# Kernel optimization log

Measured on AMD Instinct MI355X. Metric: run time of the kernel, lower is better.

The kernel has to match this reference:

```python
import jax, jax.numpy as jnp
import numpy as np

N = 13627
E = 504378
D = 500


def _seg_softmax(e, seg, n):
    m = jax.ops.segment_max(e, seg, num_segments=n)
    ex = jnp.exp(e - m[seg])
    s = jax.ops.segment_sum(ex, seg, num_segments=n)
    return ex / (s[seg] + 1e-16)


def _gatv2(x, src, dst, Wl, Wr, att, b, n):
    # PyG GATv2Conv (heads=1): message = Wl x_src; score uses Wl x_src + Wr x_dst
    xl = x @ Wl                                   # [N, F]
    xr = x @ Wr                                   # [N, F]
    e = jax.nn.leaky_relu(xl[src] + xr[dst], 0.2) @ att   # [E]
    a = _seg_softmax(e, dst, n)                   # segment softmax over targets
    out = jax.ops.segment_sum(a[:, None] * xl[src], dst, num_segments=n)
    return out + b


def setup_inputs() -> dict:
    key = jax.random.key(0)
    ks = jax.random.split(key, 24)
    s = 0.05
    inp = {
        'x': jax.random.normal(ks[0], (N, D), dtype=jnp.float32),
        'edge_index': jax.random.randint(ks[1], (2, E), 0, N),
        'neg_edge_index': jax.random.randint(ks[2], (2, E), 0, N),
        'Wl1': jax.random.normal(ks[3], (D, 300)) * s,
        'Wr1': jax.random.normal(ks[4], (D, 300)) * s,
        'att1': jax.random.normal(ks[5], (300,)) * s,
        'b1': jnp.zeros((300,)),
        'Wl2': jax.random.normal(ks[6], (300, 100)) * s,
        'Wr2': jax.random.normal(ks[7], (300, 100)) * s,
        'att2': jax.random.normal(ks[8], (100,)) * s,
        'b2': jnp.zeros((100,)),
        'Wl3': jax.random.normal(ks[9], (100, 1)) * s,
        'Wr3': jax.random.normal(ks[10], (100, 1)) * s,
        'att3': jax.random.normal(ks[11], (1,)) * s,
        'b3': jnp.zeros((1,)),
        'W_lin1': jax.random.normal(ks[12], (D, 100)) * s,
        'b_lin1': jnp.zeros((100,)),
        'W_lin2': jax.random.normal(ks[13], (D, 100)) * s,
        'b_lin2': jnp.zeros((100,)),
        'c1': jnp.array([0.5], dtype=jnp.float32),
        'c2': jnp.array([0.5], dtype=jnp.float32),
    }
    return inp


def reference(x, edge_index, neg_edge_index, Wl1, Wr1, att1, b1, Wl2, Wr2, att2, b2,
              Wl3, Wr3, att3, b3, W_lin1, b_lin1, W_lin2, b_lin2, c1, c2):
    # eval mode: dropout / dropout_adj are identity
    loops = jnp.arange(N)
    src = jnp.concatenate([edge_index[0], loops])   # GATv2Conv adds self loops
    dst = jnp.concatenate([edge_index[1], loops])

    h1 = jax.nn.relu(_gatv2(x, src, dst, Wl1, Wr1, att1, b1, N))
    h2 = jax.nn.relu(_gatv2(h1, src, dst, Wl2, Wr2, att2, b2, N))

    xo = h2 + jax.nn.relu(x @ W_lin1 + b_lin1)
    z = h2 + jax.nn.relu(x @ W_lin2 + b_lin2)

    # link-prediction reconstruction loss
    pos_s = jnp.sum(z[edge_index[0]] * z[edge_index[1]], axis=1)
    pos_loss = -jnp.mean(jnp.log(jax.nn.sigmoid(pos_s) + 1e-15))
    neg_s = jnp.sum(z[neg_edge_index[0]] * z[neg_edge_index[1]], axis=1)
    neg_loss = -jnp.mean(jnp.log(1.0 - jax.nn.sigmoid(neg_s) + 1e-15))
    r_loss = pos_loss + neg_loss

    out = _gatv2(xo, src, dst, Wl3, Wr3, att3, b3, N)   # [N, 1]
    return out, r_loss, c1, c2
```

## Files before the change

kernel.cpp:

```cpp
#include <hip/hip_runtime.h>
#include <hip/hip_bf16.h>

#define NODES 13627
#define DIM   500

typedef short short8 __attribute__((ext_vector_type(8)));
typedef float f32x4 __attribute__((ext_vector_type(4)));
typedef float floatx2 __attribute__((ext_vector_type(2)));

__device__ inline float wave_reduce_sum(float v) {
#pragma unroll
    for (int o = 32; o > 0; o >>= 1) v += __shfl_xor(v, o, 64);
    return v;
}

__device__ inline void store_v(float* p, float v) { *p = v; }
__device__ inline void store_v(__hip_bfloat16* p, float v) { *p = __float2bfloat16(v); }

__device__ inline float blo(unsigned w) { unsigned t = w << 16;        return __builtin_bit_cast(float, t); }
__device__ inline float bhi(unsigned w) { unsigned t = w & 0xffff0000u; return __builtin_bit_cast(float, t); }

__device__ inline unsigned char to_fp8(float v) {
    int r = __builtin_amdgcn_cvt_pk_fp8_f32(v, v, 0, false);
    return (unsigned char)(r & 0xff);
}

__device__ inline unsigned pk2bf(float a, float b) {
    unsigned la = (unsigned)__builtin_bit_cast(unsigned short, __float2bfloat16(a));
    unsigned hb = (unsigned)__builtin_bit_cast(unsigned short, __float2bfloat16(b));
    return la | (hb << 16);
}

template <int CTRL>
__device__ inline float dpp_add_step(float v) {
    int s = __builtin_amdgcn_update_dpp(0, __builtin_bit_cast(int, v), CTRL, 0xf, 0xf, true);
    return v + __builtin_bit_cast(float, s);
}
__device__ inline float quad16_reduce(float v) {
    v = dpp_add_step<0x128>(v);
    v = dpp_add_step<0x124>(v);
    v = dpp_add_step<0x4E>(v);
    v = dpp_add_step<0xB1>(v);
    return v;
}

struct b4 { __hip_bfloat16 a, b, c, d; };

__global__ __launch_bounds__(1024) void scan_kernel(int* __restrict__ cnt_cur,
                                                    int* __restrict__ off, int n) {
    __shared__ int wsum[16];
    const int tid = threadIdx.x, lane = tid & 63, w = tid >> 6;
    int carry = 0;
    for (int base = 0; base < n; base += 1024) {
        int i = base + tid;
        int v = (i < n) ? cnt_cur[i] : 0;
        int s = v;
#pragma unroll
        for (int o = 1; o < 64; o <<= 1) {
            int t = __shfl_up(s, o, 64);
            if (lane >= o) s += t;
        }
        if (lane == 63) wsum[w] = s;
        __syncthreads();
        if (w == 0 && lane < 16) {
            int x = wsum[lane];
            int sx = x;
#pragma unroll
            for (int o = 1; o < 16; o <<= 1) {
                int t = __shfl_up(sx, o, 64);
                if (lane >= o) sx += t;
            }
            wsum[lane] = sx;
        }
        __syncthreads();
        int wo = (w == 0) ? 0 : wsum[w - 1];
        int total = wsum[15];
        int excl = carry + wo + (s - v);
        if (i < n) { off[i] = excl; cnt_cur[i] = excl; }
        carry += total;
        __syncthreads();
    }
    if (tid == 0) off[n] = carry;
}

__global__ __launch_bounds__(256) void scatter_kernel(const int* __restrict__ src,
                                                      const int* __restrict__ dst,
                                                      int* __restrict__ cur,
                                                      int* __restrict__ ssrc, int E) {
    int i = blockIdx.x * blockDim.x + threadIdx.x;
    if (i < E) {
        int p = atomicAdd(&cur[dst[i]], 1);
        ssrc[p] = src[i];
    }
}

__global__ __launch_bounds__(256) void convert_all_kernel(
    const float* __restrict__ x,
    const float* __restrict__ Wl1, const float* __restrict__ Wr1,
    const float* __restrict__ Wl2, const float* __restrict__ Wr2,
    const float* __restrict__ Ws1, const float* __restrict__ Ws2,
    const float* __restrict__ bs1, const float* __restrict__ bs2,
    __hip_bfloat16* __restrict__ WcT, __hip_bfloat16* __restrict__ W2T,
    float* __restrict__ bcat, __hip_bfloat16* __restrict__ xb,
    const int* __restrict__ dst, int* __restrict__ cnt, int E, int M) {
    int i = blockIdx.x * 256 + threadIdx.x;
    if (i < E) atomicAdd(&cnt[dst[i]], 1);
    if (i < 327680) {
        int n = i >> 9, k = i & 511;
        float v = 0.f;
        if (k < 500) {
            if (n < 300) v = Wl1[k * 300 + n];
            else if (n < 600) v = Wr1[k * 300 + n - 300];
        }
        WcT[i] = __float2bfloat16(v);
    } else if (i < 409600) {
        int j = i - 327680;
        int n = j / 320, k = j - n * 320;
        float v = 0.f;
        if (k < 300) {
            if (n < 100) v = Wl2[k * 100 + n];
            else if (n < 200) v = Wr2[k * 100 + n - 100];
        }
        W2T[j] = __float2bfloat16(v);
    } else if (i < 540672) {
        int j = i - 409600;
        int n = j >> 9, k = j & 511;
        float v = 0.f;
        if (k < 500) {
            if (n < 100) v = Ws1[k * 100 + n];
            else if (n < 200) v = Ws2[k * 100 + n - 100];
        }
        WcT[327680 + j] = __float2bfloat16(v);
    } else if (i < 540928) {
        int n = i - 540672;
        float v = 0.f;
        if (n < 100) v = bs1[n];
        else if (n < 200) v = bs2[n - 100];
        bcat[n] = v;
    } else {
        int j = i - 540928;
        if (j >= M * 128) return;
        int m = j >> 7, k = (j & 127) << 2;
        b4 o;
        if (k < 500) {
            float4 v = *(const float4*)(x + (size_t)m * 500 + k);
            o.a = __float2bfloat16(v.x); o.b = __float2bfloat16(v.y);
            o.c = __float2bfloat16(v.z); o.d = __float2bfloat16(v.w);
        } else {
            o.a = o.b = o.c = o.d = __float2bfloat16(0.f);
        }
        *(b4*)(xb + (size_t)m * 512 + k) = o;
    }
}

template <int EPI, typename TC>
__global__ __launch_bounds__(256) void mfma_gemm(
    const __hip_bfloat16* __restrict__ A, const __hip_bfloat16* __restrict__ BT,
    TC* __restrict__ C, const float* __restrict__ bias, const float* __restrict__ h2,
    unsigned char* __restrict__ p8, __hip_bfloat16* __restrict__ pb,
    int M, int Kp, int Nn, int ldc) {
    __shared__ short AsF[8 * 64 * 8];
    __shared__ short BsF[4 * 64 * 8];
    const int t = threadIdx.x;
    const int w = t >> 6, lane = t & 63;
    const int c = t & 3, rr = t >> 2;

    const int nwg = gridDim.x * gridDim.y;
    int id = blockIdx.y * gridDim.x + blockIdx.x;
    {
        const int xcd = id & 7, idx = id >> 3;
        const int qq = nwg >> 3, r8 = nwg & 7;
        id = (xcd < r8 ? xcd * (qq + 1) : r8 * (qq + 1) + (xcd - r8) * qq) + idx;
    }
    const int m0 = (id / gridDim.x) * 128, n0 = (id % gridDim.x) * 64;

    f32x4 acc[2][4];
#pragma unroll
    for (int i = 0; i < 2; i++)
#pragma unroll
        for (int j = 0; j < 4; j++) acc[i][j] = (f32x4){0.f, 0.f, 0.f, 0.f};

    for (int k0 = 0; k0 < Kp; k0 += 32) {
#pragma unroll
        for (int r = 0; r < 2; r++) {
            int m = r * 64 + rr;
            int gm = m0 + m; if (gm >= M) gm = M - 1;
            float4 v = *(const float4*)(A + (size_t)gm * Kp + k0 + c * 8);
            int mi = m >> 4, sl = m & 15;
            *(float4*)(&AsF[(mi * 64 + c * 16 + sl) * 8]) = v;
        }
        {
            int n = rr;
            float4 v = *(const float4*)(BT + (size_t)(n0 + n) * Kp + k0 + c * 8);
            int ni = n >> 4, sl = n & 15;
            *(float4*)(&BsF[(ni * 64 + c * 16 + sl) * 8]) = v;
        }
        __syncthreads();
        short8 a0 = *(const short8*)(&AsF[((w * 2 + 0) * 64 + lane) * 8]);
        short8 a1 = *(const short8*)(&AsF[((w * 2 + 1) * 64 + lane) * 8]);
#pragma unroll
        for (int j = 0; j < 4; j++) {
            short8 b = *(const short8*)(&BsF[(j * 64 + lane) * 8]);
            acc[0][j] = __builtin_amdgcn_mfma_f32_16x16x32_bf16(a0, b, acc[0][j], 0, 0, 0);
            acc[1][j] = __builtin_amdgcn_mfma_f32_16x16x32_bf16(a1, b, acc[1][j], 0, 0, 0);
        }
        __syncthreads();
    }

    const int q = lane >> 4, sl = lane & 15;
#pragma unroll
    for (int i = 0; i < 2; i++) {
#pragma unroll
        for (int j = 0; j < 4; j++) {
#pragma unroll
            for (int reg = 0; reg < 4; reg++) {
                int gm = m0 + w * 32 + i * 16 + q * 4 + reg;
                int gn = n0 + j * 16 + sl;
                if (gm >= M) continue;
                float v = acc[i][j][reg];
                if constexpr (EPI == 1) {
                    if (gn < 300)       p8[(size_t)gm * 304 + gn] = to_fp8(v);
                    else if (gn < 600)  pb[(size_t)gm * 320 + (gn - 300)] = __float2bfloat16(v);
                    else if (gn < 620)  pb[(size_t)gm * 320 + (gn - 300)] = __float2bfloat16(0.f);
                    else if (gn < 624)  p8[(size_t)gm * 304 + (gn - 320)] = 0;
                    else if (gn >= 640 && gn < 840) {
                        int cn = gn - 640;
                        ((float*)C)[(size_t)gm * 200 + cn] = fmaxf(v + bias[cn], 0.f);
                    }
                } else if constexpr (EPI == 2) {
                    if (gn < 100)       p8[(size_t)gm * 112 + gn] = to_fp8(v);
                    else if (gn < 200)  pb[(size_t)gm * 128 + (gn - 100)] = __float2bfloat16(v);
                    else if (gn < 212)  p8[(size_t)gm * 112 + (gn - 100)] = 0;
                    else if (gn < 240)  pb[(size_t)gm * 128 + (gn - 112)] = __float2bfloat16(0.f);
                } else {
                    store_v(&C[(size_t)gm * ldc + gn], v);
                }
            }
        }
    }
}

template <int F, int NJ, int SL8, int SRB, int SOUT, int JSL, typename TOUT, bool FUSE>
__global__ __launch_bounds__(64, 4) void gat_f8_kernel(
    const unsigned char* __restrict__ xl8, const __hip_bfloat16* __restrict__ xrb,
    const float* __restrict__ att, const float* __restrict__ bias,
    const int* __restrict__ off, const int* __restrict__ ssrc,
    TOUT* __restrict__ out,
    const float* __restrict__ wpre, unsigned char* __restrict__ z8o,
    float* __restrict__ xl3, float* __restrict__ xr3,
    const float* __restrict__ wl3, const float* __restrict__ wr3, int n) {
    const int lane = threadIdx.x;
    const int sl = lane & 15, q = lane >> 4;
    const int wid = blockIdx.x;

    floatx2 attv[NJ * 2], xrv[NJ * 2], acc[NJ * 2];
    const unsigned* xru = (const unsigned*)xrb + (size_t)wid * (SRB / 2);
#pragma unroll
    for (int j = 0; j < NJ; j++) {
        const int f0 = sl * 4 + j * 64;
        if (f0 < F) {
            float4 a4 = *(const float4*)(att + f0);
            attv[j * 2 + 0] = (floatx2){a4.x, a4.y};
            attv[j * 2 + 1] = (floatx2){a4.z, a4.w};
        } else {
            attv[j * 2 + 0] = (floatx2){0.f, 0.f};
            attv[j * 2 + 1] = (floatx2){0.f, 0.f};
        }
        unsigned u0 = __builtin_nontemporal_load(xru + (f0 >> 1));
        unsigned u1 = __builtin_nontemporal_load(xru + (f0 >> 1) + 1);
        xrv[j * 2 + 0] = (floatx2){blo(u0), bhi(u0)};
        xrv[j * 2 + 1] = (floatx2){blo(u1), bhi(u1)};
        acc[j * 2 + 0] = (floatx2){0.f, 0.f};
        acc[j * 2 + 1] = (floatx2){0.f, 0.f};
    }

    const int s0 = off[wid], s1 = off[wid + 1];
    const int eb = s0 - 1;
    const int ee = s1;
    float den = 0.f;
    const int myoff = sl * 4;

    int srcB;
    unsigned u[NJ];
    {
        int eq0 = eb + q;
        int srcA = wid;
        if (eq0 >= s0 && eq0 < ee) srcA = __builtin_nontemporal_load(ssrc + eq0);
        int eq1 = eb + 4 + q;
        srcB = wid;
        if (eq1 >= s0 && eq1 < ee) srcB = __builtin_nontemporal_load(ssrc + eq1);
        const unsigned char* row = xl8 + (size_t)srcA * SL8;
#pragma unroll
        for (int j = 0; j < NJ; j++) {
            const bool ld = (j < NJ - 1) || (sl < JSL);
            u[j] = ld ? *(const unsigned*)(row + myoff + j * 64) : 0u;
        }
    }

    float p_pend = 0.f, gate = 0.f;
    unsigned u_pend[NJ];
#pragma unroll
    for (int j = 0; j < NJ; j++) u_pend[j] = 0u;

    for (int e0 = eb; e0 < ee; e0 += 4) {
        int srcC = wid;
        {
            int eq2 = e0 + 8 + q;
            if (eq2 >= s0 && eq2 < ee) srcC = __builtin_nontemporal_load(ssrc + eq2);
        }
        unsigned un[NJ];
        {
            const unsigned char* row1 = xl8 + (size_t)srcB * SL8;
#pragma unroll
            for (int j = 0; j < NJ; j++) {
                const bool ld = (j < NJ - 1) || (sl < JSL);
                un[j] = ld ? *(const unsigned*)(row1 + myoff + j * 64) : 0u;
            }
        }
        {
            float pp = quad16_reduce(p_pend);
            float ex = gate * __expf(pp);
            den += ex;
            floatx2 ex2 = (floatx2){ex, ex};
#pragma unroll
            for (int j = 0; j < NJ; j++) {
                floatx2 lo = __builtin_amdgcn_cvt_pk_f32_fp8((int)u_pend[j], false);
                floatx2 hi = __builtin_amdgcn_cvt_pk_f32_fp8((int)u_pend[j], true);
                acc[j * 2 + 0] += ex2 * lo;
                acc[j * 2 + 1] += ex2 * hi;
            }
        }
        {
            floatx2 p2 = (floatx2){0.f, 0.f};
#pragma unroll
            for (int j = 0; j < NJ; j++) {
                floatx2 lo = __builtin_amdgcn_cvt_pk_f32_fp8((int)u[j], false);
                floatx2 hi = __builtin_amdgcn_cvt_pk_f32_fp8((int)u[j], true);
                floatx2 s0v = lo + xrv[j * 2 + 0];
                floatx2 s1v = hi + xrv[j * 2 + 1];
                floatx2 g0 = __builtin_elementwise_max(s0v, 0.2f * s0v);
                floatx2 g1 = __builtin_elementwise_max(s1v, 0.2f * s1v);
                p2 += attv[j * 2 + 0] * g0;
                p2 += attv[j * 2 + 1] * g1;
            }
            p_pend = p2.x + p2.y;
            gate = ((e0 + q) < ee) ? 1.f : 0.f;
        }
#pragma unroll
        for (int j = 0; j < NJ; j++) { u_pend[j] = u[j]; u[j] = un[j]; }
        srcB = srcC;
    }
    {
        float pp = quad16_reduce(p_pend);
        float ex = gate * __expf(pp);
        den += ex;
        floatx2 ex2 = (floatx2){ex, ex};
#pragma unroll
        for (int j = 0; j < NJ; j++) {
            floatx2 lo = __builtin_amdgcn_cvt_pk_f32_fp8((int)u_pend[j], false);
            floatx2 hi = __builtin_amdgcn_cvt_pk_f32_fp8((int)u_pend[j], true);
            acc[j * 2 + 0] += ex2 * lo;
            acc[j * 2 + 1] += ex2 * hi;
        }
    }

    float* af = (float*)acc;
#pragma unroll
    for (int o = 16; o <= 32; o <<= 1) {
        den += __shfl_xor(den, o, 64);
#pragma unroll
        for (int i = 0; i < NJ * 4; i++) af[i] += __shfl_xor(af[i], o, 64);
    }

    if (q == 0) {
        const float inv = 1.f / (den + 1e-16f);
        if constexpr (FUSE) {
            float pl = 0.f, pr = 0.f;
#pragma unroll
            for (int j = 0; j < NJ; j++) {
                const int f0 = sl * 4 + j * 64;
#pragma unroll
                for (int cc = 0; cc < 4; cc++) {
                    const int f = f0 + cc;
                    if (f < F) {
                        float h2v = fmaxf(af[j * 4 + cc] * inv + bias[f], 0.f);
                        float preA = wpre[(size_t)wid * 200 + f];
                        float preB = wpre[(size_t)wid * 200 + 100 + f];
                        float xov = preA + h2v;
                        z8o[(size_t)wid * 128 + f] = to_fp8(preB + h2v);
                        pl += xov * wl3[f];
                        pr += xov * wr3[f];
                    } else {
                        z8o[(size_t)wid * 128 + f] = 0;
                    }
                }
            }
            pl = quad16_reduce(pl);
            pr = quad16_reduce(pr);
            if (sl == 0) { xl3[wid] = pl; xr3[wid] = pr; }
        } else {
#pragma unroll
            for (int j = 0; j < NJ; j++) {
                const int f0 = sl * 4 + j * 64;
                if (f0 >= SOUT) continue;
                float r[4];
#pragma unroll
                for (int cc = 0; cc < 4; cc++) {
                    const int f = f0 + cc;
                    float v = 0.f;
                    if (f < F) v = fmaxf(af[j * 4 + cc] * inv + bias[f], 0.f);
                    r[cc] = v;
                }
                if constexpr (sizeof(TOUT) == 4) {
                    *(float4*)((float*)out + (size_t)wid * SOUT + f0) =
                        make_float4(r[0], r[1], r[2], r[3]);
                } else {
                    unsigned* op = (unsigned*)out + (size_t)wid * (SOUT / 2) + (f0 >> 1);
                    op[0] = pk2bf(r[0], r[1]);
                    op[1] = pk2bf(r[2], r[3]);
                }
            }
        }
    }
}

__global__ __launch_bounds__(256) void gat3_kernel(
    const float* __restrict__ xl3, const float* __restrict__ xr3,
    const float* __restrict__ att3, const float* __restrict__ b3,
    const int* __restrict__ off, const int* __restrict__ ssrc,
    float* __restrict__ out, int n,
    const float* __restrict__ part, int nb,
    const float* __restrict__ c1, const float* __restrict__ c2, int E) {
    __shared__ float sp[4], sn[4];
    if (blockIdx.x == gridDim.x - 1) {
        const int tid = threadIdx.x, lane = tid & 63, w = tid >> 6;
        float p = 0.f, q2 = 0.f;
        for (int i = tid; i < nb; i += 256) { p += part[i]; q2 += part[nb + i]; }
        p = wave_reduce_sum(p);
        q2 = wave_reduce_sum(q2);
        if (lane == 0) { sp[w] = p; sn[w] = q2; }
        __syncthreads();
        if (tid == 0) {
            float tp = sp[0] + sp[1] + sp[2] + sp[3];
            float tq = sn[0] + sn[1] + sn[2] + sn[3];
            out[n]     = -(tp + tq) / (float)E;
            out[n + 1] = c1[0];
            out[n + 2] = c2[0];
        }
        return;
    }
    const int wid = blockIdx.x * 4 + (threadIdx.x >> 6);
    const int lane = threadIdx.x & 63;
    if (wid >= n) return;
    const float xrv = xr3[wid];
    const float att = att3[0];
    float num = 0.f, den = 0.f;
    const int s0 = off[wid], s1 = off[wid + 1];
    for (int e = s0 - 1 + lane; e < s1; e += 64) {
        int src = (e < s0) ? wid : ssrc[e];
        float xlv = xl3[src];
        float t = xlv + xrv;
        float g = t > 0.f ? t : 0.2f * t;
        float ex = __expf(g * att);
        den += ex;
        num += ex * xlv;
    }
    num = wave_reduce_sum(num);
    den = wave_reduce_sum(den);
    if (lane == 0) out[wid] = num / (den + 1e-16f) + b3[0];
}

__global__ __launch_bounds__(256) void loss_kernel(
    const unsigned char* __restrict__ z8, const int* __restrict__ pos,
    const int* __restrict__ neg, float* __restrict__ part, int nb, int E) {
    const int lane = threadIdx.x & 63;
    const int sl = lane & 15;
    const int wlocal = threadIdx.x >> 6;
    const int q = lane >> 4;
    const int nq = gridDim.x * 16;
    const int qid = (blockIdx.x * 4 + wlocal) * 4 + q;
    const int total = 2 * E;
    float psum = 0.f, nsum = 0.f;

    for (int base = qid; base < total; base += 4 * nq) {
        uint2 au[4], bu[4];
        bool act[4], isN[4];
#pragma unroll
        for (int s = 0; s < 4; s++) {
            int it = base + s * nq;
            act[s] = it < total;
            int itc = act[s] ? it : 0;
            isN[s] = itc >= E;
            int e = isN[s] ? itc - E : itc;
            const int* ei = isN[s] ? neg : pos;
            int u = ei[e], v = ei[E + e];
            au[s] = *(const uint2*)(z8 + (size_t)u * 128 + sl * 8);
            bu[s] = *(const uint2*)(z8 + (size_t)v * 128 + sl * 8);
        }
#pragma unroll
        for (int s = 0; s < 4; s++) {
            floatx2 a0 = __builtin_amdgcn_cvt_pk_f32_fp8((int)au[s].x, false);
            floatx2 a1 = __builtin_amdgcn_cvt_pk_f32_fp8((int)au[s].x, true);
            floatx2 a2 = __builtin_amdgcn_cvt_pk_f32_fp8((int)au[s].y, false);
            floatx2 a3 = __builtin_amdgcn_cvt_pk_f32_fp8((int)au[s].y, true);
            floatx2 b0 = __builtin_amdgcn_cvt_pk_f32_fp8((int)bu[s].x, false);
            floatx2 b1 = __builtin_amdgcn_cvt_pk_f32_fp8((int)bu[s].x, true);
            floatx2 b2 = __builtin_amdgcn_cvt_pk_f32_fp8((int)bu[s].y, false);
            floatx2 b3 = __builtin_amdgcn_cvt_pk_f32_fp8((int)bu[s].y, true);
            float p = a0.x * b0.x + a0.y * b0.y + a1.x * b1.x + a1.y * b1.y
                    + a2.x * b2.x + a2.y * b2.y + a3.x * b3.x + a3.y * b3.y;
            p = quad16_reduce(p);
            if (sl == 0 && act[s]) {
                float sig = __builtin_amdgcn_rcpf(1.f + __expf(-p));
                if (isN[s]) nsum += __logf(1.f - sig + 1e-15f);
                else        psum += __logf(sig + 1e-15f);
            }
        }
    }
    float pw = wave_reduce_sum(psum);
    float nw = wave_reduce_sum(nsum);
    __shared__ float sp[4], sn[4];
    if (lane == 0) { sp[wlocal] = pw; sn[wlocal] = nw; }
    __syncthreads();
    if (threadIdx.x == 0) {
        part[blockIdx.x]      = sp[0] + sp[1] + sp[2] + sp[3];
        part[nb + blockIdx.x] = sn[0] + sn[1] + sn[2] + sn[3];
    }
}

extern "C" void kernel_launch(void* const* d_in, const int* in_sizes, int n_in,
                              void* d_out, int out_size, void* d_ws, size_t ws_size,
                              hipStream_t stream) {
    const float* x      = (const float*)d_in[0];
    const int*   ei     = (const int*)d_in[1];
    const int*   nei    = (const int*)d_in[2];
    const float* Wl1    = (const float*)d_in[3];
    const float* Wr1    = (const float*)d_in[4];
    const float* att1   = (const float*)d_in[5];
    const float* b1     = (const float*)d_in[6];
    const float* Wl2    = (const float*)d_in[7];
    const float* Wr2    = (const float*)d_in[8];
    const float* att2   = (const float*)d_in[9];
    const float* b2     = (const float*)d_in[10];
    const float* Wl3    = (const float*)d_in[11];
    const float* Wr3    = (const float*)d_in[12];
    const float* att3   = (const float*)d_in[13];
    const float* b3     = (const float*)d_in[14];
    const float* Wlin1  = (const float*)d_in[15];
    const float* blin1  = (const float*)d_in[16];
    const float* Wlin2  = (const float*)d_in[17];
    const float* blin2  = (const float*)d_in[18];
    const float* c1     = (const float*)d_in[19];
    const float* c2     = (const float*)d_in[20];
    float* out = (float*)d_out;

    const int E = in_sizes[1] / 2;
    const int N = NODES;
    const int LOSS_BLOCKS = 4096;

    char* ws = (char*)d_ws;
    unsigned char*  xl8  = (unsigned char*)(ws + 0);
    unsigned char*  xl28 = (unsigned char*)(ws + 0);
    __hip_bfloat16* xrb  = (__hip_bfloat16*)(ws + 4194304);
    __hip_bfloat16* xr2b = (__hip_bfloat16*)(ws + 4194304);
    unsigned char*  z8   = (unsigned char*)(ws + 9645312);
    __hip_bfloat16* h1b  = (__hip_bfloat16*)(ws + 12915712);
    __hip_bfloat16* xb   = (__hip_bfloat16*)(ws + 21637120);
    __hip_bfloat16* WcT  = (__hip_bfloat16*)(ws + 35591168);
    __hip_bfloat16* W2T  = (__hip_bfloat16*)(ws + 36508672);
    float*          bcat = (float*)(ws + 36672512);
    float*          xl3  = (float*)(ws + 36673536);
    float*          xr3  = (float*)(ws + 36728064);
    int*            ioff = (int*)(ws + 36782592);
    int*            cur  = (int*)(ws + 36837376);
    int*            ssrc = (int*)(ws + 36892160);
    float*          part = (float*)(ws + 38909952);
    float*          wpre = (float*)(ws + 39000064);

    hipMemsetAsync(cur, 0, sizeof(int) * N, stream);

    convert_all_kernel<<<(540928 + N * 128 + 255) / 256, 256, 0, stream>>>(
        x, Wl1, Wr1, Wl2, Wr2, Wlin1, Wlin2, blin1, blin2,
        WcT, W2T, bcat, xb, ei + E, cur, E, N);

    scan_kernel<<<1, 1024, 0, stream>>>(cur, ioff, N);
    scatter_kernel<<<(E + 255) / 256, 256, 0, stream>>>(ei, ei + E, cur, ssrc, E);

    mfma_gemm<1, float><<<dim3(14, 107), 256, 0, stream>>>(
        xb, WcT, wpre, bcat, nullptr, xl8, xrb, N, 512, 896, 200);
    gat_f8_kernel<300, 5, 304, 320, 320, 11, __hip_bfloat16, false>
        <<<N, 64, 0, stream>>>(xl8, xrb, att1, b1, ioff, ssrc, h1b,
                               nullptr, nullptr, nullptr, nullptr, nullptr, nullptr, N);

    mfma_gemm<2, __hip_bfloat16><<<dim3(4, 107), 256, 0, stream>>>(
        h1b, W2T, (__hip_bfloat16*)nullptr, nullptr, nullptr, xl28, xr2b, N, 320, 256, 0);
    gat_f8_kernel<100, 2, 112, 128, 100, 9, float, true>
        <<<N, 64, 0, stream>>>(xl28, xr2b, att2, b2, ioff, ssrc, (float*)nullptr,
                               wpre, z8, xl3, xr3, Wl3, Wr3, N);

    loss_kernel<<<LOSS_BLOCKS, 256, 0, stream>>>(z8, ei, nei, part, LOSS_BLOCKS, E);

    gat3_kernel<<<(N + 3) / 4 + 1, 256, 0, stream>>>(
        xl3, xr3, att3, b3, ioff, ssrc, out, N, part, LOSS_BLOCKS, c1, c2, E);
}
```

Baseline: 327.5 us.

## Prefetch next GEMM K-tile into registers and swizzle LDS layout

The bf16 MFMA GEMM now loads the next K-slice of A and B from global memory into registers while the current slice is consumed from LDS. This overlaps global-load latency with the MFMA work. The LDS write and read positions are also XOR-like rotated by the k-chunk index, to cut bank conflicts on the float4 stores. The prefetch adds register pressure, and the GEMM is only one part of a larger pipeline dominated by edge gathers.

```diff
diff --git a/kernel.cpp b/kernel.cpp
--- a/kernel.cpp
+++ b/kernel.cpp
@@ -174,33 +174,49 @@
     }
     const int m0 = (id / gridDim.x) * 128, n0 = (id % gridDim.x) * 64;
 
+    const int slw = rr & 15;
+    const int miw = rr >> 4;
+    const int posw = c * 16 + ((slw + 4 * c) & 15);
+    const int kc = lane >> 4, rl = lane & 15;
+    const int posr = kc * 16 + ((rl + 4 * kc) & 15);
+
+    int gmA[2];
+#pragma unroll
+    for (int r = 0; r < 2; r++) {
+        int gm = m0 + r * 64 + rr;
+        gmA[r] = (gm >= M) ? (M - 1) : gm;
+    }
+    const int gnB = n0 + rr;
+
     f32x4 acc[2][4];
 #pragma unroll
     for (int i = 0; i < 2; i++)
 #pragma unroll
         for (int j = 0; j < 4; j++) acc[i][j] = (f32x4){0.f, 0.f, 0.f, 0.f};
 
+    float4 ra[2], rbv;
+#pragma unroll
+    for (int r = 0; r < 2; r++)
+        ra[r] = *(const float4*)(A + (size_t)gmA[r] * Kp + c * 8);
+    rbv = *(const float4*)(BT + (size_t)gnB * Kp + c * 8);
+
     for (int k0 = 0; k0 < Kp; k0 += 32) {
 #pragma unroll
-        for (int r = 0; r < 2; r++) {
-            int m = r * 64 + rr;
-            int gm = m0 + m; if (gm >= M) gm = M - 1;
-            float4 v = *(const float4*)(A + (size_t)gm * Kp + k0 + c * 8);
-            int mi = m >> 4, sl = m & 15;
-            *(float4*)(&AsF[(mi * 64 + c * 16 + sl) * 8]) = v;
-        }
-        {
-            int n = rr;
-            float4 v = *(const float4*)(BT + (size_t)(n0 + n) * Kp + k0 + c * 8);
-            int ni = n >> 4, sl = n & 15;
-            *(float4*)(&BsF[(ni * 64 + c * 16 + sl) * 8]) = v;
-        }
+        for (int r = 0; r < 2; r++)
+            *(float4*)(&AsF[((r * 4 + miw) * 64 + posw) * 8]) = ra[r];
+        *(float4*)(&BsF[(miw * 64 + posw) * 8]) = rbv;
         __syncthreads();
-        short8 a0 = *(const short8*)(&AsF[((w * 2 + 0) * 64 + lane) * 8]);
-        short8 a1 = *(const short8*)(&AsF[((w * 2 + 1) * 64 + lane) * 8]);
+        if (k0 + 32 < Kp) {
+#pragma unroll
+            for (int r = 0; r < 2; r++)
+                ra[r] = *(const float4*)(A + (size_t)gmA[r] * Kp + k0 + 32 + c * 8);
+            rbv = *(const float4*)(BT + (size_t)gnB * Kp + k0 + 32 + c * 8);
+        }
+        short8 a0 = *(const short8*)(&AsF[((w * 2 + 0) * 64 + posr) * 8]);
+        short8 a1 = *(const short8*)(&AsF[((w * 2 + 1) * 64 + posr) * 8]);
 #pragma unroll
         for (int j = 0; j < 4; j++) {
-            short8 b = *(const short8*)(&BsF[(j * 64 + lane) * 8]);
+            short8 b = *(const short8*)(&BsF[(j * 64 + posr) * 8]);
             acc[0][j] = __builtin_amdgcn_mfma_f32_16x16x32_bf16(a0, b, acc[0][j], 0, 0, 0);
             acc[1][j] = __builtin_amdgcn_mfma_f32_16x16x32_bf16(a1, b, acc[1][j], 0, 0, 0);
         }
```

Result: slower. 373.0 us (+13.9%).
